# Kernel tuning notes

Hardware: AMD Instinct MI355X
Metric: run time of the kernel (lower is better)

The kernel has to match this reference:

```python
import jax, jax.numpy as jnp
import numpy as np

N_T, N_C, N_D = 500_000, 200_000, 100_000  # target / card / device node counts
E = 1_000_000                              # edges per relation
IN, HID, OUT = 64, 64, 2


def setup_inputs() -> dict:
    key = jax.random.key(0)
    ks = jax.random.split(key, 18)
    f32 = jnp.float32
    inp = {
        "features": jax.random.normal(ks[0], (N_T, IN), f32),
        "emb_card": jax.random.normal(ks[1], (N_C, IN), f32) * 0.05,
        "emb_device": jax.random.normal(ks[2], (N_D, IN), f32) * 0.05,
        "W1": jax.random.normal(ks[3], (4, IN, HID), f32) * 0.05,
        "b1": jax.random.normal(ks[4], (4, HID), f32) * 0.05,
        "W2": jax.random.normal(ks[5], (4, HID, HID), f32) * 0.05,
        "b2": jax.random.normal(ks[6], (4, HID), f32) * 0.05,
        "W_out": jax.random.normal(ks[7], (HID, OUT), f32) * 0.05,
        "b_out": jax.random.normal(ks[8], (OUT,), f32) * 0.05,
        "src_c2t": jax.random.randint(ks[9], (E,), 0, N_C, jnp.int32),
        "dst_c2t": jax.random.randint(ks[10], (E,), 0, N_T, jnp.int32),
        "src_t2c": jax.random.randint(ks[11], (E,), 0, N_T, jnp.int32),
        "dst_t2c": jax.random.randint(ks[12], (E,), 0, N_C, jnp.int32),
        "src_d2t": jax.random.randint(ks[13], (E,), 0, N_D, jnp.int32),
        "dst_d2t": jax.random.randint(ks[14], (E,), 0, N_T, jnp.int32),
        "src_t2d": jax.random.randint(ks[15], (E,), 0, N_T, jnp.int32),
        "dst_t2d": jax.random.randint(ks[16], (E,), 0, N_D, jnp.int32),
    }
    return inp


def _mean_agg(Wh, src, dst, n_dst):
    """copy_u gather + scatter-mean: mean over incoming edges of Wh[src]."""
    msgs = Wh[src]  # [E, H] gather
    s = jax.ops.segment_sum(msgs, dst, num_segments=n_dst)
    deg = jax.ops.segment_sum(jnp.ones((src.shape[0],), Wh.dtype), dst, num_segments=n_dst)
    return s / jnp.maximum(deg, 1.0)[:, None]  # zero in-degree -> 0 (DGL default)


def _layer(x_t, x_c, x_d, W, b, edges):
    # etype order: 0 card->target, 1 target->card, 2 device->target, 3 target->device
    (sc2t, dc2t, st2c, dt2c, sd2t, dd2t, st2d, dt2d) = edges
    Wh0 = x_c @ W[0] + b[0]
    Wh1 = x_t @ W[1] + b[1]
    Wh2 = x_d @ W[2] + b[2]
    Wh3 = x_t @ W[3] + b[3]
    # cross-relation reducer = 'sum'
    h_t = _mean_agg(Wh0, sc2t, dc2t, N_T) + _mean_agg(Wh2, sd2t, dd2t, N_T)
    h_c = _mean_agg(Wh1, st2c, dt2c, N_C)
    h_d = _mean_agg(Wh3, st2d, dt2d, N_D)
    return h_t, h_c, h_d


def reference(features, emb_card, emb_device, W1, b1, W2, b2, W_out, b_out,
              src_c2t, dst_c2t, src_t2c, dst_t2c, src_d2t, dst_d2t, src_t2d, dst_t2d):
    edges = (src_c2t, dst_c2t, src_t2c, dst_t2c, src_d2t, dst_d2t, src_t2d, dst_t2d)
    h_t, h_c, h_d = _layer(features, emb_card, emb_device, W1, b1, edges)
    h_t, h_c, h_d = (jax.nn.leaky_relu(h, 0.01) for h in (h_t, h_c, h_d))
    h_t, h_c, h_d = _layer(h_t, h_c, h_d, W2, b2, edges)
    return h_t @ W_out + b_out  # [N_T, OUT] logits for target node type
```

## Files before the change

### kernel.cpp

```cpp
#include <hip/hip_runtime.h>
#include <hip/hip_bf16.h>


#define NT 500000
#define NC 200000
#define ND 100000
#define NE 1000000
#define H  64
#define CAP_T2C 32
#define CAP_T2D 48

#define PACK_SCALE 65536.0f
#define PACK_BIAS  262144
#define FIELD_MASK 0x3FFFFFFULL

#define NBK_MAX 489
#define NBK2 489
#define OFF_C2T 196
#define OFF_D2T 685
#define EPB 4096
#define BPR 245
#define CAP_BK1 11776
#define CAP_BK2 2688

#define CB512 7813

__device__ __forceinline__ void rel_params(int rel, int& shift, int& hoff, int& nbk) {
    shift = (rel == 0) ? 11 : 10;
    hoff = (rel == 0) ? 0 : (rel == 1) ? 98 : (rel == 2) ? OFF_C2T : OFF_D2T;
    nbk = (rel < 2) ? 98 : NBK2;
}

#define BFP(x) (u = __float_as_uint(x), (u + 0x7fffu + ((u >> 16) & 1u)) >> 16)

__global__ __launch_bounds__(512)
void scatter_compress(const int* __restrict__ st2c, const int* __restrict__ dt2c,
                      const int* __restrict__ st2d, const int* __restrict__ dt2d,
                      const int* __restrict__ sc2t, const int* __restrict__ dc2t,
                      const int* __restrict__ sd2t, const int* __restrict__ dd2t,
                      int* __restrict__ cur,
                      unsigned long long* __restrict__ bedges1,
                      unsigned long long* __restrict__ bedges2,
                      const float* __restrict__ X, unsigned int* __restrict__ Xb,
                      const float* __restrict__ W2, const float* __restrict__ b2,
                      const float* __restrict__ Wout,
                      float* __restrict__ Wc, float* __restrict__ bc) {
    __shared__ unsigned long long le[EPB];
    __shared__ int h[NBK_MAX], pref[NBK_MAX], gbase[NBK_MAX], csr[NBK_MAX];
    __shared__ int sc[512];
    int t = threadIdx.x, b = blockIdx.x;

    if (b >= 4 * BPR) {
        int cb = b - 4 * BPR;
        if (cb < CB512) {
            size_t idx = (size_t)cb * 512 + t;
            if (idx < 4000000) {
                const float4 f0 = ((const float4*)X)[idx * 2];
                const float4 f1 = ((const float4*)X)[idx * 2 + 1];
                uint4 o;
                unsigned int u;
                o.x = BFP(f0.x) | (BFP(f0.y) << 16);
                o.y = BFP(f0.z) | (BFP(f0.w) << 16);
                o.z = BFP(f1.x) | (BFP(f1.y) << 16);
                o.w = BFP(f1.z) | (BFP(f1.w) << 16);
                ((uint4*)Xb)[idx] = o;
            }
        } else if (t < 256) {
            int rel = t >> 7;
            int rem = t & 127;
            int k = rem >> 1, o = rem & 1;
            const float* W2r = W2 + (rel ? 2 : 0) * H * H;
            float s = 0.0f;
            for (int j = 0; j < H; ++j) s += W2r[k * H + j] * Wout[j * 2 + o];
            Wc[rel * 128 + k * 2 + o] = s;
            if (rem < 4) {
                int r2 = rem >> 1, o2 = rem & 1;
                const float* b2r = b2 + (r2 ? 2 : 0) * H;
                float sb = 0.0f;
                for (int j = 0; j < H; ++j) sb += b2r[j] * Wout[j * 2 + o2];
                bc[r2 * 2 + o2] = sb;
            }
        }
        return;
    }

    int rel = b / BPR;
    int bb = b - rel * BPR;
    const int* sp = (rel == 0) ? st2c : (rel == 1) ? st2d : (rel == 2) ? sc2t : sd2t;
    const int* dp = (rel == 0) ? dt2c : (rel == 1) ? dt2d : (rel == 2) ? dc2t : dd2t;
    int shift, hoff, nbk;
    rel_params(rel, shift, hoff, nbk);
    unsigned long long* bedges = (rel < 2) ? bedges1 : bedges2;
    int bkoff = (rel == 1) ? 98 : (rel == 3) ? NBK2 : 0;
    int bkcap = (rel < 2) ? CAP_BK1 : CAP_BK2;

    for (int i = t; i < nbk; i += 512) { h[i] = 0; csr[i] = 0; }
    __syncthreads();

    int base = bb * EPB + t * 8;
    bool ok = base < NE;
    int4 d0, d1, s0, s1;
    if (ok) {
        d0 = *(const int4*)(dp + base);
        d1 = *(const int4*)(dp + base + 4);
        s0 = *(const int4*)(sp + base);
        s1 = *(const int4*)(sp + base + 4);
        atomicAdd(&h[d0.x >> shift], 1);
        atomicAdd(&h[d0.y >> shift], 1);
        atomicAdd(&h[d0.z >> shift], 1);
        atomicAdd(&h[d0.w >> shift], 1);
        atomicAdd(&h[d1.x >> shift], 1);
        atomicAdd(&h[d1.y >> shift], 1);
        atomicAdd(&h[d1.z >> shift], 1);
        atomicAdd(&h[d1.w >> shift], 1);
    }
    __syncthreads();
    if (t < nbk && h[t]) gbase[t] = (bkoff + t) * bkcap + atomicAdd(&cur[hoff + t], h[t]);
    sc[t] = (t < nbk) ? h[t] : 0;
    __syncthreads();
    for (int s = 1; s < 512; s <<= 1) {
        int y = (t >= s) ? sc[t - s] : 0;
        __syncthreads();
        sc[t] += y;
        __syncthreads();
    }
    if (t < nbk) pref[t] = sc[t] - h[t];
    __syncthreads();

    if (ok) {
        #define BIN(dv, sv) { int k = (dv) >> shift; \
            int l = atomicAdd(&csr[k], 1); \
            le[pref[k] + l] = ((unsigned long long)(unsigned int)(dv) << 32) | (unsigned int)(sv); }
        BIN(d0.x, s0.x) BIN(d0.y, s0.y) BIN(d0.z, s0.z) BIN(d0.w, s0.w)
        BIN(d1.x, s1.x) BIN(d1.y, s1.y) BIN(d1.z, s1.z) BIN(d1.w, s1.w)
        #undef BIN
    }
    __syncthreads();

    int n_e = NE - bb * EPB; if (n_e > EPB) n_e = EPB;
    for (int i = t; i < n_e; i += 512) {
        unsigned long long e = le[i];
        int k = (int)(e >> 32) >> shift;
        bedges[(size_t)gbase[k] + (i - pref[k])] = e;
    }
}

__global__ __launch_bounds__(1024)
void radix_build(const unsigned long long* __restrict__ bedges1, const int* __restrict__ cur,
                 int* __restrict__ cnt_t2c, int* __restrict__ cols_t2c,
                 int* __restrict__ cnt_t2d, int* __restrict__ cols_t2d) {
    __shared__ int lc[2048];
    int t = threadIdx.x, k = blockIdx.x;
    int rel = k >= 98 ? 1 : 0;
    int shift = rel ? 10 : 11;
    int range = 1 << shift;
    int noff = (rel ? (k - 98) : k) << shift;
    int nN = rel ? ND : NC;
    int* cnt = rel ? cnt_t2d : cnt_t2c;
    int* cols = rel ? cols_t2d : cols_t2c;
    int cap = rel ? CAP_T2D : CAP_T2C;
    int e0 = k * CAP_BK1;
    int e1 = e0 + cur[k];
    for (int i = t; i < range; i += 1024) lc[i] = 0;
    __syncthreads();
    for (int i = e0 + t; i < e1; i += 1024) {
        unsigned long long e = bedges1[i];
        int d = (int)(e >> 32);
        int s = (int)(e & 0xffffffffu);
        int l = atomicAdd(&lc[d - noff], 1);
        if (l < cap) cols[(size_t)d * cap + l] = s;
    }
    __syncthreads();
    for (int i = t; i < range; i += 1024) {
        int gn = noff + i;
        if (gn < nN) cnt[gn] = lc[i];
    }
}

#define NBGM_C 3125
#define NBGM_D 1563

__global__ __launch_bounds__(512)
void gather_mean(const unsigned int* __restrict__ Xb,
                 const int* __restrict__ cnt_c, const int* __restrict__ cols_c,
                 const int* __restrict__ cnt_d, const int* __restrict__ cols_d,
                 unsigned int* __restrict__ mB) {
    int t = threadIdx.x;
    int lane = t & 63;
    int w = t >> 6;
    int half = lane >> 5;
    int li = lane & 31;

    int bn, nNodes, cap;
    const int* cnt; const int* cols; unsigned int* mP;
    if (blockIdx.x < NBGM_C) {
        bn = blockIdx.x * 64; nNodes = NC; cap = CAP_T2C;
        cnt = cnt_c; cols = cols_c; mP = mB;
    } else {
        bn = (blockIdx.x - NBGM_C) * 64; nNodes = ND; cap = CAP_T2D;
        cnt = cnt_d; cols = cols_d; mP = mB + (size_t)NC * 32;
    }

    int gnb = bn + w * 8;
    int cval = 0;
    if (lane < 8 && gnb + lane < nNodes) cval = cnt[gnb + lane];

    int cc[8], mm[8], cv[8];
#pragma unroll
    for (int r = 0; r < 8; ++r) {
        cc[r] = __shfl(cval, r);
        mm[r] = cc[r] < cap ? cc[r] : cap;
    }
#pragma unroll
    for (int r = 0; r < 8; ++r) {
        int gn = gnb + r;
        cv[r] = (lane < mm[r] && gn < nNodes) ? cols[(size_t)gn * cap + lane] : 0;
    }

    int maxm = 0;
#pragma unroll
    for (int r = 0; r < 8; ++r) maxm = maxm > mm[r] ? maxm : mm[r];

    float ax[8], ay[8];
#pragma unroll
    for (int r = 0; r < 8; ++r) { ax[r] = 0.0f; ay[r] = 0.0f; }

    for (int j = 0; j < maxm; j += 2) {
#pragma unroll
        for (int r = 0; r < 8; ++r) {
            int sA = __shfl(cv[r], j);
            int sB = __shfl(cv[r], j + 1);
            int src = half ? sB : sA;
            unsigned int v = 0;
            if (j + half < mm[r]) v = Xb[(size_t)src * 32 + li];
            ax[r] += __uint_as_float(v << 16);
            ay[r] += __uint_as_float(v & 0xffff0000u);
        }
    }

#pragma unroll
    for (int r = 0; r < 8; ++r) {
        float fx = ax[r] + __shfl_xor(ax[r], 32);
        float fy = ay[r] + __shfl_xor(ay[r], 32);
        float inv = cc[r] > 0 ? 1.0f / (float)cc[r] : 0.0f;
        ax[r] = fx * inv; ay[r] = fy * inv;
    }
    unsigned int u;
#pragma unroll
    for (int r = 0; r < 8; r += 2) {
        int gn = gnb + r + half;
        float vx = half ? ax[r + 1] : ax[r];
        float vy = half ? ay[r + 1] : ay[r];
        unsigned int pv = BFP(vx) | (BFP(vy) << 16);
        if (gn < nNodes) mP[(size_t)gn * 32 + li] = pv;
    }
}

#define NBX_C 3125
#define NBX_D 1563

__global__ __launch_bounds__(256)
void xform_tile(const unsigned int* __restrict__ mB,
                const int* __restrict__ cnt_c, const int* __restrict__ cnt_d,
                const float* __restrict__ W1, const float* __restrict__ b1,
                const float* __restrict__ Wc, const float* __restrict__ bc,
                float* __restrict__ Pc, float* __restrict__ Pd) {
    __shared__ float Xt[64][68];
    __shared__ float Wl[64][68];
    __shared__ float msk[64];
    int t = threadIdx.x;

    int bn, nNodes; const unsigned int* mrow; const int* cnt;
    const float* W1r; const float* b1r; const float* Wcr; const float* bcr;
    float* P;
    if (blockIdx.x < NBX_C) {
        bn = blockIdx.x * 64; nNodes = NC;
        mrow = mB; cnt = cnt_c;
        W1r = W1 + 1 * H * H; b1r = b1 + 1 * H; Wcr = Wc; bcr = bc; P = Pc;
    } else {
        bn = (blockIdx.x - NBX_C) * 64; nNodes = ND;
        mrow = mB + (size_t)NC * 32; cnt = cnt_d;
        W1r = W1 + 3 * H * H; b1r = b1 + 3 * H; Wcr = Wc + 128; bcr = bc + 2; P = Pd;
    }

    {
        int node = t & 63, seg = t >> 6;
        int gn = bn + node;
        uint4 v0 = make_uint4(0, 0, 0, 0), v1 = make_uint4(0, 0, 0, 0);
        if (gn < nNodes) {
            const uint4* rp = (const uint4*)(mrow + (size_t)gn * 32);
            v0 = rp[seg * 2];
            v1 = rp[seg * 2 + 1];
        }
        int k0 = seg * 16;
        Xt[k0 + 0][node] = __uint_as_float(v0.x << 16);
        Xt[k0 + 1][node] = __uint_as_float(v0.x & 0xffff0000u);
        Xt[k0 + 2][node] = __uint_as_float(v0.y << 16);
        Xt[k0 + 3][node] = __uint_as_float(v0.y & 0xffff0000u);
        Xt[k0 + 4][node] = __uint_as_float(v0.z << 16);
        Xt[k0 + 5][node] = __uint_as_float(v0.z & 0xffff0000u);
        Xt[k0 + 6][node] = __uint_as_float(v0.w << 16);
        Xt[k0 + 7][node] = __uint_as_float(v0.w & 0xffff0000u);
        Xt[k0 + 8][node] = __uint_as_float(v1.x << 16);
        Xt[k0 + 9][node] = __uint_as_float(v1.x & 0xffff0000u);
        Xt[k0 + 10][node] = __uint_as_float(v1.y << 16);
        Xt[k0 + 11][node] = __uint_as_float(v1.y & 0xffff0000u);
        Xt[k0 + 12][node] = __uint_as_float(v1.z << 16);
        Xt[k0 + 13][node] = __uint_as_float(v1.z & 0xffff0000u);
        Xt[k0 + 14][node] = __uint_as_float(v1.w << 16);
        Xt[k0 + 15][node] = __uint_as_float(v1.w & 0xffff0000u);
        for (int q = t; q < 1024; q += 256) {
            int kk = q >> 4, s2 = q & 15;
            *(float4*)&Wl[kk][s2 * 4] = *(const float4*)(W1r + kk * H + s2 * 4);
        }
        if (t < 64) msk[t] = (bn + t < nNodes && cnt[bn + t] > 0) ? 1.0f : 0.0f;
    }
    __syncthreads();

    int tj = t & 15;
    int ti = t >> 4;
    float4 b4 = *(const float4*)(b1r + tj * 4);
    float a4[4][4];
#pragma unroll
    for (int r = 0; r < 4; ++r) {
        a4[r][0] = b4.x; a4[r][1] = b4.y; a4[r][2] = b4.z; a4[r][3] = b4.w;
    }
#pragma unroll
    for (int k = 0; k < H; ++k) {
        float4 a = *(const float4*)&Xt[k][ti * 4];
        float4 b = *(const float4*)&Wl[k][tj * 4];
        a4[0][0] = fmaf(a.x, b.x, a4[0][0]); a4[0][1] = fmaf(a.x, b.y, a4[0][1]);
        a4[0][2] = fmaf(a.x, b.z, a4[0][2]); a4[0][3] = fmaf(a.x, b.w, a4[0][3]);
        a4[1][0] = fmaf(a.y, b.x, a4[1][0]); a4[1][1] = fmaf(a.y, b.y, a4[1][1]);
        a4[1][2] = fmaf(a.y, b.z, a4[1][2]); a4[1][3] = fmaf(a.y, b.w, a4[1][3]);
        a4[2][0] = fmaf(a.z, b.x, a4[2][0]); a4[2][1] = fmaf(a.z, b.y, a4[2][1]);
        a4[2][2] = fmaf(a.z, b.z, a4[2][2]); a4[2][3] = fmaf(a.z, b.w, a4[2][3]);
        a4[3][0] = fmaf(a.w, b.x, a4[3][0]); a4[3][1] = fmaf(a.w, b.y, a4[3][1]);
        a4[3][2] = fmaf(a.w, b.z, a4[3][2]); a4[3][3] = fmaf(a.w, b.w, a4[3][3]);
    }

    float4 wca = *(const float4*)(Wcr + tj * 8);
    float4 wcb = *(const float4*)(Wcr + tj * 8 + 4);
    float p0[4], p1[4];
#pragma unroll
    for (int r = 0; r < 4; ++r) {
        float m = msk[ti * 4 + r];
        float h0 = a4[r][0], h1 = a4[r][1], h2 = a4[r][2], h3 = a4[r][3];
        h0 = (h0 > 0.f ? h0 : 0.01f * h0) * m;
        h1 = (h1 > 0.f ? h1 : 0.01f * h1) * m;
        h2 = (h2 > 0.f ? h2 : 0.01f * h2) * m;
        h3 = (h3 > 0.f ? h3 : 0.01f * h3) * m;
        p0[r] = h0 * wca.x + h1 * wca.z + h2 * wcb.x + h3 * wcb.z;
        p1[r] = h0 * wca.y + h1 * wca.w + h2 * wcb.y + h3 * wcb.w;
    }
#pragma unroll
    for (int off = 1; off < 16; off <<= 1) {
#pragma unroll
        for (int r = 0; r < 4; ++r) {
            p0[r] += __shfl_xor(p0[r], off);
            p1[r] += __shfl_xor(p1[r], off);
        }
    }
    if (tj == 0) {
#pragma unroll
        for (int r = 0; r < 4; ++r) {
            int gn = bn + ti * 4 + r;
            if (gn < nNodes) {
                float2 o = make_float2(p0[r] + bcr[0], p1[r] + bcr[1]);
                *(float2*)(P + 2 * (size_t)gn) = o;
            }
        }
    }
}

__device__ __forceinline__ unsigned long long pack_p(const float* __restrict__ P, int s) {
    float2 pv = *(const float2*)(P + 2 * (size_t)s);
    float a = fminf(fmaxf(pv.x, -3.99f), 3.99f);
    float b = fminf(fmaxf(pv.y, -3.99f), 3.99f);
    unsigned int ia = (unsigned int)(__float2int_rn(a * PACK_SCALE) + PACK_BIAS);
    unsigned int ib = (unsigned int)(__float2int_rn(b * PACK_SCALE) + PACK_BIAS);
    return (1ULL << 52) | ((unsigned long long)ia << 26) | (unsigned long long)ib;
}

__global__ __launch_bounds__(512)
void agg_out(const unsigned long long* __restrict__ bedges2, const int* __restrict__ cur,
             const float* __restrict__ Pc, const float* __restrict__ Pd,
             const float* __restrict__ bout, float* __restrict__ out) {
    __shared__ unsigned long long accC[1024], accD[1024];
    int t = threadIdx.x, k = blockIdx.x;
    int noff = k << 10;
    int range = NT - noff; if (range > 1024) range = 1024;
    for (int i = t; i < 1024; i += 512) { accC[i] = 0ULL; accD[i] = 0ULL; }
    __syncthreads();

    int e0 = k * CAP_BK2, e1 = e0 + cur[OFF_C2T + k];
    for (int i = e0 + t; i < e1; i += 512) {
        unsigned long long e = bedges2[i];
        int d = (int)(e >> 32);
        int s = (int)(e & 0xffffffffu);
        atomicAdd(&accC[d - noff], pack_p(Pc, s));
    }
    int f0 = (NBK2 + k) * CAP_BK2, f1 = f0 + cur[OFF_D2T + k];
    for (int i = f0 + t; i < f1; i += 512) {
        unsigned long long e = bedges2[i];
        int d = (int)(e >> 32);
        int s = (int)(e & 0xffffffffu);
        atomicAdd(&accD[d - noff], pack_p(Pd, s));
    }
    __syncthreads();

    float bo0 = bout[0], bo1 = bout[1];
    const float inv_s = 1.0f / PACK_SCALE;
    for (int i = t; i < range; i += 512) {
        unsigned long long xc = accC[i];
        unsigned long long xd = accD[i];
        int dc = (int)(xc >> 52);
        int dd = (int)(xd >> 52);
        float ic = dc > 0 ? 1.0f / (float)dc : 0.0f;
        float id = dd > 0 ? 1.0f / (float)dd : 0.0f;
        float c0 = (float)((long long)((xc >> 26) & FIELD_MASK) - (long long)dc * PACK_BIAS);
        float c1 = (float)((long long)(xc & FIELD_MASK) - (long long)dc * PACK_BIAS);
        float d0 = (float)((long long)((xd >> 26) & FIELD_MASK) - (long long)dd * PACK_BIAS);
        float d1 = (float)((long long)(xd & FIELD_MASK) - (long long)dd * PACK_BIAS);
        float2 o;
        o.x = bo0 + (c0 * ic + d0 * id) * inv_s;
        o.y = bo1 + (c1 * ic + d1 * id) * inv_s;
        *(float2*)(out + 2 * (size_t)(noff + i)) = o;
    }
}

extern "C" void kernel_launch(void* const* d_in, const int* in_sizes, int n_in,
                              void* d_out, int out_size, void* d_ws, size_t ws_size,
                              hipStream_t stream) {
    const float* features = (const float*)d_in[0];
    const float* W1 = (const float*)d_in[3];
    const float* b1 = (const float*)d_in[4];
    const float* W2 = (const float*)d_in[5];
    const float* b2 = (const float*)d_in[6];
    const float* W_out = (const float*)d_in[7];
    const float* b_out = (const float*)d_in[8];
    const int* src_c2t = (const int*)d_in[9];
    const int* dst_c2t = (const int*)d_in[10];
    const int* src_t2c = (const int*)d_in[11];
    const int* dst_t2c = (const int*)d_in[12];
    const int* src_d2t = (const int*)d_in[13];
    const int* dst_d2t = (const int*)d_in[14];
    const int* src_t2d = (const int*)d_in[15];
    const int* dst_t2d = (const int*)d_in[16];
    float* out = (float*)d_out;

    char* w = (char*)d_ws;
    int* cur = (int*)w;                           w += 2048 * 4;
    size_t zero_bytes = 2048 * 4;
    int* cnt_t2c = (int*)w;                       w += (size_t)NC * 4;
    int* cnt_t2d = (int*)w;                       w += (size_t)ND * 4;
    int* cols_t2c = (int*)w;                      w += (size_t)NC * CAP_T2C * 4;
    int* cols_t2d = (int*)w;                      w += (size_t)ND * CAP_T2D * 4;
    float* p_c = (float*)w;                       w += (size_t)NC * 2 * 4;
    float* p_d = (float*)w;                       w += (size_t)ND * 2 * 4;
    float* Wc = (float*)w;                        w += 256 * 4;
    float* bc = (float*)w;                        w += 16;
    unsigned long long* bedges1 = (unsigned long long*)w;  w += (size_t)196 * CAP_BK1 * 8;
    unsigned long long* bedges2 = (unsigned long long*)w;  w += (size_t)(2 * NBK2) * CAP_BK2 * 8;
    unsigned int* Xb = (unsigned int*)w;          w += (size_t)NT * H * 2;
    unsigned int* mB = (unsigned int*)w;          w += ((size_t)(NC + ND) + 64) * 32 * 4;

    hipMemsetAsync(d_ws, 0, zero_bytes, stream);

    scatter_compress<<<4 * BPR + CB512 + 1, 512, 0, stream>>>(
        src_t2c, dst_t2c, src_t2d, dst_t2d,
        src_c2t, dst_c2t, src_d2t, dst_d2t,
        cur, bedges1, bedges2,
        features, Xb, W2, b2, W_out, Wc, bc);

    radix_build<<<196, 1024, 0, stream>>>(bedges1, cur,
                                          cnt_t2c, cols_t2c, cnt_t2d, cols_t2d);

    gather_mean<<<NBGM_C + NBGM_D, 512, 0, stream>>>(
        Xb, cnt_t2c, cols_t2c, cnt_t2d, cols_t2d, mB);

    xform_tile<<<NBX_C + NBX_D, 256, 0, stream>>>(
        mB, cnt_t2c, cnt_t2d, W1, b1, Wc, bc, p_c, p_d);

    agg_out<<<NBK2, 512, 0, stream>>>(bedges2, cur, p_c, p_d, b_out, out);
}
```

Baseline: 229.4 us.

## Pack bucketed edges into 32-bit words and move c2t/d2t binning into gather kernel

Bucketed edges are now stored as one 32-bit word holding a 13-bit local destination and a 19-bit source, replacing the 64-bit pair. This halves the global write and read traffic for the edge buckets in radix_build and agg_out. The scatter for the card/device-to-target relations moves out of the first kernel and into the gather_mean launch. That shortens the critical path before radix_build and lets the binning overlap with the gather work. The block prefix scan now uses wavefront shuffles instead of a barrier-heavy shared-memory scan, which adds a dependence on the packed field widths fitting the node ranges.

```diff
diff --git a/kernel.cpp b/kernel.cpp
--- a/kernel.cpp
+++ b/kernel.cpp
@@ -25,72 +25,23 @@
 
 #define CB512 7813
 
-__device__ __forceinline__ void rel_params(int rel, int& shift, int& hoff, int& nbk) {
-    shift = (rel == 0) ? 11 : 10;
-    hoff = (rel == 0) ? 0 : (rel == 1) ? 98 : (rel == 2) ? OFF_C2T : OFF_D2T;
-    nbk = (rel < 2) ? 98 : NBK2;
-}
+#define NBGM_C 3125
+#define NBGM_D 1563
+#define NBX_C 3125
+#define NBX_D 1563
 
 #define BFP(x) (u = __float_as_uint(x), (u + 0x7fffu + ((u >> 16) & 1u)) >> 16)
 
-__global__ __launch_bounds__(512)
-void scatter_compress(const int* __restrict__ st2c, const int* __restrict__ dt2c,
-                      const int* __restrict__ st2d, const int* __restrict__ dt2d,
-                      const int* __restrict__ sc2t, const int* __restrict__ dc2t,
-                      const int* __restrict__ sd2t, const int* __restrict__ dd2t,
-                      int* __restrict__ cur,
-                      unsigned long long* __restrict__ bedges1,
-                      unsigned long long* __restrict__ bedges2,
-                      const float* __restrict__ X, unsigned int* __restrict__ Xb,
-                      const float* __restrict__ W2, const float* __restrict__ b2,
-                      const float* __restrict__ Wout,
-                      float* __restrict__ Wc, float* __restrict__ bc) {
-    __shared__ unsigned long long le[EPB];
-    __shared__ int h[NBK_MAX], pref[NBK_MAX], gbase[NBK_MAX], csr[NBK_MAX];
-    __shared__ int sc[512];
-    int t = threadIdx.x, b = blockIdx.x;
-
-    if (b >= 4 * BPR) {
-        int cb = b - 4 * BPR;
-        if (cb < CB512) {
-            size_t idx = (size_t)cb * 512 + t;
-            if (idx < 4000000) {
-                const float4 f0 = ((const float4*)X)[idx * 2];
-                const float4 f1 = ((const float4*)X)[idx * 2 + 1];
-                uint4 o;
-                unsigned int u;
-                o.x = BFP(f0.x) | (BFP(f0.y) << 16);
-                o.y = BFP(f0.z) | (BFP(f0.w) << 16);
-                o.z = BFP(f1.x) | (BFP(f1.y) << 16);
-                o.w = BFP(f1.z) | (BFP(f1.w) << 16);
-                ((uint4*)Xb)[idx] = o;
-            }
-        } else if (t < 256) {
-            int rel = t >> 7;
-            int rem = t & 127;
-            int k = rem >> 1, o = rem & 1;
-            const float* W2r = W2 + (rel ? 2 : 0) * H * H;
-            float s = 0.0f;
-            for (int j = 0; j < H; ++j) s += W2r[k * H + j] * Wout[j * 2 + o];
-            Wc[rel * 128 + k * 2 + o] = s;
-            if (rem < 4) {
-                int r2 = rem >> 1, o2 = rem & 1;
-                const float* b2r = b2 + (r2 ? 2 : 0) * H;
-                float sb = 0.0f;
-                for (int j = 0; j < H; ++j) sb += b2r[j] * Wout[j * 2 + o2];
-                bc[r2 * 2 + o2] = sb;
-            }
-        }
-        return;
-    }
-
-    int rel = b / BPR;
-    int bb = b - rel * BPR;
-    const int* sp = (rel == 0) ? st2c : (rel == 1) ? st2d : (rel == 2) ? sc2t : sd2t;
-    const int* dp = (rel == 0) ? dt2c : (rel == 1) ? dt2d : (rel == 2) ? dc2t : dd2t;
-    int shift, hoff, nbk;
-    rel_params(rel, shift, hoff, nbk);
-    unsigned long long* bedges = (rel < 2) ? bedges1 : bedges2;
+__device__ __forceinline__ void scatter_body(
+        const int* __restrict__ sp, const int* __restrict__ dp,
+        int bb, int rel, int* __restrict__ cur, unsigned int* __restrict__ bedges,
+        unsigned long long* le, int* h, int* pref, int* gbase, int* csr,
+        int* wsum, int* woff) {
+    int t = threadIdx.x;
+    int lane = t & 63, w = t >> 6;
+    int shift = (rel == 0) ? 11 : 10;
+    int nbk = (rel < 2) ? 98 : NBK2;
+    int hoff = (rel == 0) ? 0 : (rel == 1) ? 98 : (rel == 2) ? OFF_C2T : OFF_D2T;
     int bkoff = (rel == 1) ? 98 : (rel == 3) ? NBK2 : 0;
     int bkcap = (rel < 2) ? CAP_BK1 : CAP_BK2;
 
@@ -115,16 +66,24 @@
         atomicAdd(&h[d1.w >> shift], 1);
     }
     __syncthreads();
-    if (t < nbk && h[t]) gbase[t] = (bkoff + t) * bkcap + atomicAdd(&cur[hoff + t], h[t]);
-    sc[t] = (t < nbk) ? h[t] : 0;
-    __syncthreads();
-    for (int s = 1; s < 512; s <<= 1) {
-        int y = (t >= s) ? sc[t - s] : 0;
-        __syncthreads();
-        sc[t] += y;
-        __syncthreads();
-    }
-    if (t < nbk) pref[t] = sc[t] - h[t];
+
+    int hv = (t < nbk) ? h[t] : 0;
+    if (t < nbk && hv) gbase[t] = (bkoff + t) * bkcap + atomicAdd(&cur[hoff + t], hv);
+    int v = hv;
+#pragma unroll
+    for (int d = 1; d < 64; d <<= 1) {
+        int y = __shfl_up(v, d);
+        v += (lane >= d) ? y : 0;
+    }
+    if (lane == 63) wsum[w] = v;
+    __syncthreads();
+    if (t < 8) {
+        int s = 0;
+        for (int j = 0; j < t; ++j) s += wsum[j];
+        woff[t] = s;
+    }
+    __syncthreads();
+    if (t < nbk) pref[t] = v - hv + woff[w];
     __syncthreads();
 
     if (ok) {
@@ -140,13 +99,69 @@
     int n_e = NE - bb * EPB; if (n_e > EPB) n_e = EPB;
     for (int i = t; i < n_e; i += 512) {
         unsigned long long e = le[i];
-        int k = (int)(e >> 32) >> shift;
-        bedges[(size_t)gbase[k] + (i - pref[k])] = e;
+        unsigned int dst = (unsigned int)(e >> 32);
+        unsigned int srcv = (unsigned int)e;
+        int k = dst >> shift;
+        unsigned int packed = ((dst - ((unsigned int)k << shift)) << 19) | srcv;
+        bedges[(size_t)gbase[k] + (i - pref[k])] = packed;
+    }
+}
+
+__global__ __launch_bounds__(512)
+void scatter01_compress(const int* __restrict__ st2c, const int* __restrict__ dt2c,
+                        const int* __restrict__ st2d, const int* __restrict__ dt2d,
+                        int* __restrict__ cur, unsigned int* __restrict__ bedges1,
+                        const float* __restrict__ X, unsigned int* __restrict__ Xb,
+                        const float* __restrict__ W2, const float* __restrict__ b2,
+                        const float* __restrict__ Wout,
+                        float* __restrict__ Wc, float* __restrict__ bc) {
+    __shared__ unsigned long long le[EPB];
+    __shared__ int h[NBK_MAX], pref[NBK_MAX], gbase[NBK_MAX], csr[NBK_MAX];
+    __shared__ int wsum[8], woff[8];
+    int t = threadIdx.x, b = blockIdx.x;
+
+    if (b < 2 * BPR) {
+        int rel = b / BPR;
+        int bb = b - rel * BPR;
+        const int* sp = (rel == 0) ? st2c : st2d;
+        const int* dp = (rel == 0) ? dt2c : dt2d;
+        scatter_body(sp, dp, bb, rel, cur, bedges1, le, h, pref, gbase, csr, wsum, woff);
+        return;
+    }
+    int cb = b - 2 * BPR;
+    if (cb < CB512) {
+        size_t idx = (size_t)cb * 512 + t;
+        if (idx < 4000000) {
+            const float4 f0 = ((const float4*)X)[idx * 2];
+            const float4 f1 = ((const float4*)X)[idx * 2 + 1];
+            uint4 o;
+            unsigned int u;
+            o.x = BFP(f0.x) | (BFP(f0.y) << 16);
+            o.y = BFP(f0.z) | (BFP(f0.w) << 16);
+            o.z = BFP(f1.x) | (BFP(f1.y) << 16);
+            o.w = BFP(f1.z) | (BFP(f1.w) << 16);
+            ((uint4*)Xb)[idx] = o;
+        }
+    } else if (t < 256) {
+        int rel = t >> 7;
+        int rem = t & 127;
+        int k = rem >> 1, o = rem & 1;
+        const float* W2r = W2 + (rel ? 2 : 0) * H * H;
+        float s = 0.0f;
+        for (int j = 0; j < H; ++j) s += W2r[k * H + j] * Wout[j * 2 + o];
+        Wc[rel * 128 + k * 2 + o] = s;
+        if (rem < 4) {
+            int r2 = rem >> 1, o2 = rem & 1;
+            const float* b2r = b2 + (r2 ? 2 : 0) * H;
+            float sb = 0.0f;
+            for (int j = 0; j < H; ++j) sb += b2r[j] * Wout[j * 2 + o2];
+            bc[r2 * 2 + o2] = sb;
+        }
     }
 }
 
 __global__ __launch_bounds__(1024)
-void radix_build(const unsigned long long* __restrict__ bedges1, const int* __restrict__ cur,
+void radix_build(const unsigned int* __restrict__ bedges1, const int* __restrict__ cur,
                  int* __restrict__ cnt_t2c, int* __restrict__ cols_t2c,
                  int* __restrict__ cnt_t2d, int* __restrict__ cols_t2d) {
     __shared__ int lc[2048];
@@ -164,11 +179,11 @@
     for (int i = t; i < range; i += 1024) lc[i] = 0;
     __syncthreads();
     for (int i = e0 + t; i < e1; i += 1024) {
-        unsigned long long e = bedges1[i];
-        int d = (int)(e >> 32);
-        int s = (int)(e & 0xffffffffu);
-        int l = atomicAdd(&lc[d - noff], 1);
-        if (l < cap) cols[(size_t)d * cap + l] = s;
+        unsigned int e = bedges1[i];
+        int dloc = e >> 19;
+        int s = e & 0x7FFFF;
+        int l = atomicAdd(&lc[dloc], 1);
+        if (l < cap) cols[(size_t)(noff + dloc) * cap + l] = s;
     }
     __syncthreads();
     for (int i = t; i < range; i += 1024) {
@@ -177,15 +192,29 @@
     }
 }
 
-#define NBGM_C 3125
-#define NBGM_D 1563
-
 __global__ __launch_bounds__(512)
-void gather_mean(const unsigned int* __restrict__ Xb,
-                 const int* __restrict__ cnt_c, const int* __restrict__ cols_c,
-                 const int* __restrict__ cnt_d, const int* __restrict__ cols_d,
-                 unsigned int* __restrict__ mB) {
-    int t = threadIdx.x;
+void gather_scatter23(const unsigned int* __restrict__ Xb,
+                      const int* __restrict__ cnt_c, const int* __restrict__ cols_c,
+                      const int* __restrict__ cnt_d, const int* __restrict__ cols_d,
+                      unsigned int* __restrict__ mB,
+                      const int* __restrict__ sc2t, const int* __restrict__ dc2t,
+                      const int* __restrict__ sd2t, const int* __restrict__ dd2t,
+                      int* __restrict__ cur, unsigned int* __restrict__ bedges2) {
+    __shared__ unsigned long long le[EPB];
+    __shared__ int h[NBK_MAX], pref[NBK_MAX], gbase[NBK_MAX], csr[NBK_MAX];
+    __shared__ int wsum[8], woff[8];
+    int t = threadIdx.x, b = blockIdx.x;
+
+    if (b < 2 * BPR) {
+        int rel = 2 + b / BPR;
+        int bb = b - (rel - 2) * BPR;
+        const int* sp = (rel == 2) ? sc2t : sd2t;
+        const int* dp = (rel == 2) ? dc2t : dd2t;
+        scatter_body(sp, dp, bb, rel, cur, bedges2, le, h, pref, gbase, csr, wsum, woff);
+        return;
+    }
+
+    int gb = b - 2 * BPR;
     int lane = t & 63;
     int w = t >> 6;
     int half = lane >> 5;
@@ -193,11 +222,11 @@
 
     int bn, nNodes, cap;
     const int* cnt; const int* cols; unsigned int* mP;
-    if (blockIdx.x < NBGM_C) {
-        bn = blockIdx.x * 64; nNodes = NC; cap = CAP_T2C;
+    if (gb < NBGM_C) {
+        bn = gb * 64; nNodes = NC; cap = CAP_T2C;
         cnt = cnt_c; cols = cols_c; mP = mB;
     } else {
-        bn = (blockIdx.x - NBGM_C) * 64; nNodes = ND; cap = CAP_T2D;
+        bn = (gb - NBGM_C) * 64; nNodes = ND; cap = CAP_T2D;
         cnt = cnt_d; cols = cols_d; mP = mB + (size_t)NC * 32;
     }
 
@@ -255,9 +284,6 @@
         if (gn < nNodes) mP[(size_t)gn * 32 + li] = pv;
     }
 }
-
-#define NBX_C 3125
-#define NBX_D 1563
 
 __global__ __launch_bounds__(256)
 void xform_tile(const unsigned int* __restrict__ mB,
@@ -383,7 +409,7 @@
 }
 
 __global__ __launch_bounds__(512)
-void agg_out(const unsigned long long* __restrict__ bedges2, const int* __restrict__ cur,
+void agg_out(const unsigned int* __restrict__ bedges2, const int* __restrict__ cur,
              const float* __restrict__ Pc, const float* __restrict__ Pd,
              const float* __restrict__ bout, float* __restrict__ out) {
     __shared__ unsigned long long accC[1024], accD[1024];
@@ -395,17 +421,17 @@
 
     int e0 = k * CAP_BK2, e1 = e0 + cur[OFF_C2T + k];
     for (int i = e0 + t; i < e1; i += 512) {
-        unsigned long long e = bedges2[i];
-        int d = (int)(e >> 32);
-        int s = (int)(e & 0xffffffffu);
-        atomicAdd(&accC[d - noff], pack_p(Pc, s));
+        unsigned int e = bedges2[i];
+        int dloc = e >> 19;
+        int s = e & 0x7FFFF;
+        atomicAdd(&accC[dloc], pack_p(Pc, s));
     }
     int f0 = (NBK2 + k) * CAP_BK2, f1 = f0 + cur[OFF_D2T + k];
     for (int i = f0 + t; i < f1; i += 512) {
-        unsigned long long e = bedges2[i];
-        int d = (int)(e >> 32);
-        int s = (int)(e & 0xffffffffu);
-        atomicAdd(&accD[d - noff], pack_p(Pd, s));
+        unsigned int e = bedges2[i];
+        int dloc = e >> 19;
+        int s = e & 0x7FFFF;
+        atomicAdd(&accD[dloc], pack_p(Pd, s));
     }
     __syncthreads();
 
@@ -460,24 +486,23 @@
     float* p_d = (float*)w;                       w += (size_t)ND * 2 * 4;
     float* Wc = (float*)w;                        w += 256 * 4;
     float* bc = (float*)w;                        w += 16;
-    unsigned long long* bedges1 = (unsigned long long*)w;  w += (size_t)196 * CAP_BK1 * 8;
-    unsigned long long* bedges2 = (unsigned long long*)w;  w += (size_t)(2 * NBK2) * CAP_BK2 * 8;
+    unsigned int* bedges1 = (unsigned int*)w;     w += (size_t)196 * CAP_BK1 * 4;
+    unsigned int* bedges2 = (unsigned int*)w;     w += (size_t)(2 * NBK2) * CAP_BK2 * 4;
     unsigned int* Xb = (unsigned int*)w;          w += (size_t)NT * H * 2;
     unsigned int* mB = (unsigned int*)w;          w += ((size_t)(NC + ND) + 64) * 32 * 4;
 
     hipMemsetAsync(d_ws, 0, zero_bytes, stream);
 
-    scatter_compress<<<4 * BPR + CB512 + 1, 512, 0, stream>>>(
+    scatter01_compress<<<2 * BPR + CB512 + 1, 512, 0, stream>>>(
         src_t2c, dst_t2c, src_t2d, dst_t2d,
-        src_c2t, dst_c2t, src_d2t, dst_d2t,
-        cur, bedges1, bedges2,
-        features, Xb, W2, b2, W_out, Wc, bc);
+        cur, bedges1, features, Xb, W2, b2, W_out, Wc, bc);
 
     radix_build<<<196, 1024, 0, stream>>>(bedges1, cur,
                                           cnt_t2c, cols_t2c, cnt_t2d, cols_t2d);
 
-    gather_mean<<<NBGM_C + NBGM_D, 512, 0, stream>>>(
-        Xb, cnt_t2c, cols_t2c, cnt_t2d, cols_t2d, mB);
+    gather_scatter23<<<2 * BPR + NBGM_C + NBGM_D, 512, 0, stream>>>(
+        Xb, cnt_t2c, cols_t2c, cnt_t2d, cols_t2d, mB,
+        src_c2t, dst_c2t, src_d2t, dst_d2t, cur, bedges2);
 
     xform_tile<<<NBX_C + NBX_D, 256, 0, stream>>>(
         mB, cnt_t2c, cnt_t2d, W1, b1, Wc, bc, p_c, p_d);
```

After: 222.6 us (median of 2 runs). 1.03x faster.
